# Optimization experiments

Measured on AMD Instinct MI355X. Metric: run time of the kernel, lower is better.

## Reference

```python
import jax, jax.numpy as jnp
import numpy as np

HEADS = 4
NEG_SLOPE = 0.2  # DGL GATConv default leaky_relu slope


def _gat_conv(h, src, dst, W, al, ar, resW, b, heads, out_feats, num_nodes):
    """DGL GATConv semantics with prefix-shape support.
    h: [N, *prefix, in]; returns [N, *prefix, heads, out_feats].
    """
    prefix = h.shape[1:-1]
    z = jnp.einsum('...i,ij->...j', h, W).reshape(h.shape[0], *prefix, heads, out_feats)
    # per-node attention halves: [N, *prefix, heads, 1]
    el = jnp.sum(z * al, axis=-1, keepdims=True)
    er = jnp.sum(z * ar, axis=-1, keepdims=True)
    # per-edge logits: [E, *prefix, heads, 1]
    e = jax.nn.leaky_relu(el[src] + er[dst], NEG_SLOPE)
    # edge softmax over incoming edges of each dst node (stable)
    emax = jax.ops.segment_max(e, dst, num_segments=num_nodes)
    emax = jax.lax.stop_gradient(jnp.where(jnp.isfinite(emax), emax, 0.0))
    ex = jnp.exp(e - emax[dst])
    denom = jax.ops.segment_sum(ex, dst, num_segments=num_nodes)
    a = ex / jnp.where(denom == 0, 1.0, denom)[dst]
    # weighted scatter-aggregate of messages
    rst = jax.ops.segment_sum(z[src] * a, dst, num_segments=num_nodes)
    # residual projection + bias + relu activation
    res = jnp.einsum('...i,ij->...j', h, resW).reshape(h.shape[0], *prefix, heads, out_feats)
    return jax.nn.relu(rst + res + b.reshape(heads, out_feats))


def setup_inputs() -> dict:
    key = jax.random.key(0)
    ks = jax.random.split(key, 16)
    N, E, IN, HID, OUT2, CLS = 8192, 65536, 256, 512, 32, 40
    def w(k, shape, fan_in):
        return jax.random.normal(k, shape, dtype=jnp.float32) * (1.0 / np.sqrt(fan_in))
    return {
        'features': jax.random.normal(ks[0], (N, IN), dtype=jnp.float32),
        'src': jax.random.randint(ks[1], (E,), 0, N, dtype=jnp.int32),
        'dst': jax.random.randint(ks[2], (E,), 0, N, dtype=jnp.int32),
        # layer 1: in=256 -> heads=4, out=512
        'W1': w(ks[3], (IN, HEADS * HID), IN),
        'al1': w(ks[4], (HEADS, HID), HID),
        'ar1': w(ks[5], (HEADS, HID), HID),
        'resW1': w(ks[6], (IN, HEADS * HID), IN),
        'b1': jnp.zeros((HEADS * HID,), dtype=jnp.float32),
        # layer 2: in=512 -> heads=4, out=32 (applied per prefix head dim)
        'W2': w(ks[7], (HID, HEADS * OUT2), HID),
        'al2': w(ks[8], (HEADS, OUT2), OUT2),
        'ar2': w(ks[9], (HEADS, OUT2), OUT2),
        'resW2': w(ks[10], (HID, HEADS * OUT2), HID),
        'b2': jnp.zeros((HEADS * OUT2,), dtype=jnp.float32),
        # final linear: 32*4^2 = 512 -> 40
        'Wout': w(ks[11], (OUT2 * HEADS * HEADS, CLS), OUT2 * HEADS * HEADS),
        'bout': jnp.zeros((CLS,), dtype=jnp.float32),
    }


def reference(features, src, dst, W1, al1, ar1, resW1, b1, W2, al2, ar2, resW2, b2, Wout, bout):
    N = features.shape[0]
    # dropout is identity at inference
    h1 = _gat_conv(features, src, dst, W1, al1, ar1, resW1, b1, HEADS, 512, N)  # [N,4,512]
    h2 = _gat_conv(h1, src, dst, W2, al2, ar2, resW2, b2, HEADS, 32, N)        # [N,4,4,32]
    h = h2.reshape(N, -1)  # [N,512]
    return h @ Wout + bout
```

## Files before the change

### kernel.cpp

```cpp
#include <hip/hip_runtime.h>
#include <cmath>

constexpr int IN_F  = 256;

typedef short bf16x8 __attribute__((ext_vector_type(8)));
typedef short short4v __attribute__((ext_vector_type(4)));
typedef float f32x4 __attribute__((ext_vector_type(4)));

__device__ __forceinline__ short f2bf(float f) {
    unsigned u = __float_as_uint(f);
    unsigned r = (u + 0x7FFFu + ((u >> 16) & 1)) >> 16;
    return (short)r;
}
__device__ __forceinline__ float b2f(short s) {
    return __uint_as_float(((unsigned)(unsigned short)s) << 16);
}

__device__ __forceinline__ int xcd_logical_id()
{
    int nx = gridDim.x, ny = gridDim.y, nz = gridDim.z;
    int flat = blockIdx.x + nx * (blockIdx.y + ny * blockIdx.z);
    int nwg = nx * ny * nz;
    if (nwg & 7) return flat;
    int chunk = nwg >> 3;
    return (flat & 7) * chunk + (flat >> 3);
}

__device__ __forceinline__ void cvt_t_body(
    const float* __restrict__ W, short* __restrict__ Wt, int K, int N,
    int ldwt, int koff, int bk, int bn, int tx, int ty)
{
    __shared__ float tile[32][33];
    for (int i = ty; i < 32; i += 8) {
        int gn = bn + tx;
        tile[i][tx] = (gn < N) ? W[(size_t)(bk + i) * N + gn] : 0.f;
    }
    __syncthreads();
    for (int i = ty; i < 32; i += 8)
        Wt[(size_t)(bn + i) * ldwt + koff + bk + tx] = f2bf(tile[tx][i]);
}

__global__ __launch_bounds__(256) void prep_all(
    const float* __restrict__ W1, const float* __restrict__ al1, const float* __restrict__ ar1,
    const float* __restrict__ resW1, const float* __restrict__ resW2,
    const float* __restrict__ W2, const float* __restrict__ Wout, const float* __restrict__ b2,
    short* __restrict__ Wcomb, short* __restrict__ W2comb, short* __restrict__ Wtout,
    float* __restrict__ wal1, float* __restrict__ war1,
    float* __restrict__ bias2c, int* __restrict__ zero_base)
{
    int bid = blockIdx.x;
    int t   = threadIdx.x;
    if (bid < 256) {
        int wid  = (bid * 256 + t) >> 6;
        int lane = t & 63;
        int k = wid >> 2, h = wid & 3;
        const float* wr  = W1  + (size_t)k * 2048 + h * 512;
        const float* alp = al1 + h * 512;
        const float* arp = ar1 + h * 512;
        float sl = 0.f, sr = 0.f;
        for (int j = lane; j < 512; j += 64) {
            float wv = wr[j];
            sl = fmaf(wv, alp[j], sl);
            sr = fmaf(wv, arp[j], sr);
        }
#pragma unroll
        for (int o = 32; o; o >>= 1) { sl += __shfl_down(sl, o); sr += __shfl_down(sr, o); }
        if (lane == 0) { wal1[wid] = sl; war1[wid] = sr; }
    } else if (bid < 1280) {
        int id = bid - 256;
        int bx = id & 63, by = (id >> 6) & 7, bz = id >> 9;
        const float* W = bz ? resW1 : W1;
        cvt_t_body(W, Wcomb, 256, 2048, 512, bz ? 256 : 0,
                   by * 32, bx * 32, t & 31, t >> 5);
    } else if (bid < 1472) {
        int id = bid - 1280;
        int bx = id & 3, by = (id >> 2) & 15, bz = id >> 6;
        const float* W; short* Wt; int N;
        if (bz == 0)      { W = W2;    Wt = W2comb;             N = 128; }
        else if (bz == 1) { W = resW2; Wt = W2comb + 128 * 512; N = 128; }
        else              { W = Wout;  Wt = Wtout;              N = 40;  }
        cvt_t_body(W, Wt, 512, N, 512, 0, by * 32, bx * 32, t & 31, t >> 5);
    } else if (bid == 1472) {
        bias2c[t] = (t < 128) ? 0.f : b2[t - 128];
    } else {
        int b = bid - 1473;
        int4 z; z.x = 0; z.y = 0; z.z = 0; z.w = 0;
        ((int4*)zero_base)[(size_t)b * 256 + t] = z;
    }
}

__global__ __launch_bounds__(256) void l1_front(
    const float* __restrict__ feat, const float4* __restrict__ wal, const float4* __restrict__ war,
    short* __restrict__ featb, float* __restrict__ el, float* __restrict__ er,
    const int* __restrict__ dst, int* __restrict__ deg, int E, int nfeat)
{
    if ((int)blockIdx.x >= nfeat) {
        int e = (blockIdx.x - nfeat) * 256 + threadIdx.x;
        if (e < E) atomicAdd(&deg[dst[e]], 1);
        return;
    }
    int row  = blockIdx.x * 4 + (threadIdx.x >> 6);
    int lane = threadIdx.x & 63;
    float4 v = ((const float4*)feat)[(size_t)row * 64 + lane];
    short4v o;
    o[0] = f2bf(v.x); o[1] = f2bf(v.y); o[2] = f2bf(v.z); o[3] = f2bf(v.w);
    *(short4v*)(featb + (size_t)row * 256 + lane * 4) = o;

    float fj[4] = { v.x, v.y, v.z, v.w };
    int k = lane * 4;
    float sl[4] = {}, sr[4] = {};
#pragma unroll
    for (int j = 0; j < 4; j++) {
        float4 wl = wal[k + j], wr = war[k + j];
        sl[0] = fmaf(fj[j], wl.x, sl[0]); sl[1] = fmaf(fj[j], wl.y, sl[1]);
        sl[2] = fmaf(fj[j], wl.z, sl[2]); sl[3] = fmaf(fj[j], wl.w, sl[3]);
        sr[0] = fmaf(fj[j], wr.x, sr[0]); sr[1] = fmaf(fj[j], wr.y, sr[1]);
        sr[2] = fmaf(fj[j], wr.z, sr[2]); sr[3] = fmaf(fj[j], wr.w, sr[3]);
    }
#pragma unroll
    for (int o2 = 32; o2; o2 >>= 1) {
#pragma unroll
        for (int h = 0; h < 4; h++) { sl[h] += __shfl_down(sl[h], o2); sr[h] += __shfl_down(sr[h], o2); }
    }
    if (lane == 0) {
#pragma unroll
        for (int h = 0; h < 4; h++) { el[row * 4 + h] = sl[h]; er[row * 4 + h] = sr[h]; }
    }
}

__global__ __launch_bounds__(256) void el2_from_z2(
    const short* __restrict__ z2res, const float* __restrict__ al2, const float* __restrict__ ar2,
    float* __restrict__ el, float* __restrict__ er)
{
    int m    = blockIdx.x * 4 + (threadIdx.x >> 6);
    int lane = threadIdx.x & 63;
    unsigned zv = *(const unsigned*)(z2res + (size_t)m * 256 + lane * 2);
    float z0 = b2f((short)(zv & 0xFFFFu)), z1 = b2f((short)(zv >> 16));
    int c = lane >> 4;
    int j = (lane & 15) * 2;
    float sl = fmaf(z1, al2[c * 32 + j + 1], z0 * al2[c * 32 + j]);
    float sr = fmaf(z1, ar2[c * 32 + j + 1], z0 * ar2[c * 32 + j]);
#pragma unroll
    for (int o = 8; o; o >>= 1) { sl += __shfl_xor(sl, o); sr += __shfl_xor(sr, o); }
    if ((lane & 15) == 0) { el[m * 4 + c] = sl; er[m * 4 + c] = sr; }
}

__global__ __launch_bounds__(256) void gemm_bf16(
    const short* __restrict__ A, const short* __restrict__ Bt,
    const float* __restrict__ bias, void* __restrict__ C,
    int M, int N, int K, int ldc, int nmax, int out_bf16)
{
    __shared__ short sA[2][128 * 32];
    __shared__ short sB[2][128 * 32];
    const int tid  = threadIdx.x;
    const int wave = tid >> 6, lane = tid & 63;
    const int wm = wave >> 1, wn = wave & 1;
    int lid = xcd_logical_id();
    const int bx = lid % gridDim.x, by = lid / gridDim.x;
    const int m0 = by * 128, n0 = bx * 128;

    const int srow = tid >> 2;
    const int scol = (tid & 3) * 8;
    const int fr = lane & 15;
    const int fq = lane >> 4;

    f32x4 acc[4][4] = {};

    for (int k0 = 0; k0 < K; k0 += 64) {
#pragma unroll
        for (int hh = 0; hh < 2; hh++) {
            int kc = k0 + hh * 32 + scol;
            const short* ga0 = A  + (size_t)(m0 + srow) * K + kc;
            const short* ga1 = A  + (size_t)(m0 + 64 + srow) * K + kc;
            const short* gb0 = Bt + (size_t)(n0 + srow) * K + kc;
            const short* gb1 = Bt + (size_t)(n0 + 64 + srow) * K + kc;
            __builtin_amdgcn_global_load_lds((const __attribute__((address_space(1))) void*)ga0,
                (__attribute__((address_space(3))) void*)(sA[hh] + wave * 512), 16, 0, 0);
            __builtin_amdgcn_global_load_lds((const __attribute__((address_space(1))) void*)ga1,
                (__attribute__((address_space(3))) void*)(sA[hh] + 2048 + wave * 512), 16, 0, 0);
            __builtin_amdgcn_global_load_lds((const __attribute__((address_space(1))) void*)gb0,
                (__attribute__((address_space(3))) void*)(sB[hh] + wave * 512), 16, 0, 0);
            __builtin_amdgcn_global_load_lds((const __attribute__((address_space(1))) void*)gb1,
                (__attribute__((address_space(3))) void*)(sB[hh] + 2048 + wave * 512), 16, 0, 0);
        }
        __syncthreads();

#pragma unroll
        for (int hh = 0; hh < 2; hh++) {
            bf16x8 af[4], bfr[4];
#pragma unroll
            for (int m = 0; m < 4; m++)
                af[m] = *(const bf16x8*)(sA[hh] + (wm * 64 + m * 16 + fr) * 32 + fq * 8);
#pragma unroll
            for (int n = 0; n < 4; n++)
                bfr[n] = *(const bf16x8*)(sB[hh] + (wn * 64 + n * 16 + fr) * 32 + fq * 8);
#pragma unroll
            for (int m = 0; m < 4; m++)
#pragma unroll
                for (int n = 0; n < 4; n++)
                    acc[m][n] = __builtin_amdgcn_mfma_f32_16x16x32_bf16(af[m], bfr[n], acc[m][n], 0, 0, 0);
        }
        __syncthreads();
    }

#pragma unroll
    for (int n = 0; n < 4; n++) {
        int gcol = n0 + wn * 64 + n * 16 + fr;
        if (gcol >= nmax) continue;
        float bv = bias ? bias[gcol] : 0.f;
#pragma unroll
        for (int m = 0; m < 4; m++) {
#pragma unroll
            for (int j = 0; j < 4; j++) {
                int grow = m0 + wm * 64 + m * 16 + fq * 4 + j;
                float v = acc[m][n][j] + bv;
                if (out_bf16) ((short*)C)[(size_t)grow * ldc + gcol] = f2bf(v);
                else          ((float*)C)[(size_t)grow * ldc + gcol] = v;
            }
        }
    }
}

__global__ __launch_bounds__(256) void gemm_h1(
    const short* __restrict__ Acomb, const short* __restrict__ Wcomb,
    const float* __restrict__ b1, short* __restrict__ h1b)
{
    __shared__ short sA[2][128 * 32];
    __shared__ short sB[2][128 * 32];
    const int tid  = threadIdx.x;
    const int wave = tid >> 6, lane = tid & 63;
    const int wm = wave >> 1, wn = wave & 1;
    int lid = xcd_logical_id();
    const int bx = lid & 3;
    const int by = (lid >> 2) % gridDim.y;
    const int h  = lid / (gridDim.y * 4);
    const int m0 = by * 128, n0 = bx * 128;
    const short* A  = Acomb + h * 512;
    const short* Bt = Wcomb + (size_t)(h * 512) * 512;

    const int srow = tid >> 2;
    const int scol = (tid & 3) * 8;
    const int fr = lane & 15;
    const int fq = lane >> 4;

    f32x4 acc[4][4] = {};

    for (int k0 = 0; k0 < 512; k0 += 64) {
#pragma unroll
        for (int hh = 0; hh < 2; hh++) {
            int kc = k0 + hh * 32 + scol;
            const short* ga0 = A  + (size_t)(m0 + srow) * 2048 + kc;
            const short* ga1 = A  + (size_t)(m0 + 64 + srow) * 2048 + kc;
            const short* gb0 = Bt + (size_t)(n0 + srow) * 512 + kc;
            const short* gb1 = Bt + (size_t)(n0 + 64 + srow) * 512 + kc;
            __builtin_amdgcn_global_load_lds((const __attribute__((address_space(1))) void*)ga0,
                (__attribute__((address_space(3))) void*)(sA[hh] + wave * 512), 16, 0, 0);
            __builtin_amdgcn_global_load_lds((const __attribute__((address_space(1))) void*)ga1,
                (__attribute__((address_space(3))) void*)(sA[hh] + 2048 + wave * 512), 16, 0, 0);
            __builtin_amdgcn_global_load_lds((const __attribute__((address_space(1))) void*)gb0,
                (__attribute__((address_space(3))) void*)(sB[hh] + wave * 512), 16, 0, 0);
            __builtin_amdgcn_global_load_lds((const __attribute__((address_space(1))) void*)gb1,
                (__attribute__((address_space(3))) void*)(sB[hh] + 2048 + wave * 512), 16, 0, 0);
        }
        __syncthreads();

#pragma unroll
        for (int hh = 0; hh < 2; hh++) {
            bf16x8 af[4], bfr[4];
#pragma unroll
            for (int m = 0; m < 4; m++)
                af[m] = *(const bf16x8*)(sA[hh] + (wm * 64 + m * 16 + fr) * 32 + fq * 8);
#pragma unroll
            for (int n = 0; n < 4; n++)
                bfr[n] = *(const bf16x8*)(sB[hh] + (wn * 64 + n * 16 + fr) * 32 + fq * 8);
#pragma unroll
            for (int m = 0; m < 4; m++)
#pragma unroll
                for (int n = 0; n < 4; n++)
                    acc[m][n] = __builtin_amdgcn_mfma_f32_16x16x32_bf16(af[m], bfr[n], acc[m][n], 0, 0, 0);
        }
        __syncthreads();
    }

#pragma unroll
    for (int n = 0; n < 4; n++) {
        int gcol = h * 512 + n0 + wn * 64 + n * 16 + fr;
        float bv = b1[gcol];
#pragma unroll
        for (int m = 0; m < 4; m++) {
#pragma unroll
            for (int j = 0; j < 4; j++) {
                int grow = m0 + wm * 64 + m * 16 + fq * 4 + j;
                float v = acc[m][n][j] + bv;
                h1b[(size_t)grow * 2048 + gcol] = f2bf(v > 0.f ? v : 0.f);
            }
        }
    }
}

__global__ __launch_bounds__(1024) void scan_excl(const int* __restrict__ deg,
                                                  int* __restrict__ off, int N)
{
    __shared__ int part[1024];
    int t = threadIdx.x;
    int chunk = N >> 10;
    int base = t * chunk;
    int local[16];
    int s = 0;
    for (int i = 0; i < chunk; i++) { local[i] = s; s += deg[base + i]; }
    part[t] = s;
    __syncthreads();
    for (int o = 1; o < 1024; o <<= 1) {
        int v = (t >= o) ? part[t - o] : 0;
        __syncthreads();
        part[t] += v;
        __syncthreads();
    }
    int pre = (t == 0) ? 0 : part[t - 1];
    for (int i = 0; i < chunk; i++) off[base + i] = pre + local[i];
    if (t == 1023) off[N] = pre + s;
}

__global__ void scatter_kernel(const int* __restrict__ dst, const int* __restrict__ off,
                               int* __restrict__ cur, int* __restrict__ eid, int E)
{
    int e = blockIdx.x * blockDim.x + threadIdx.x;
    if (e < E) {
        int d = dst[e];
        int p = off[d] + atomicAdd(&cur[d], 1);
        eid[p] = e;
    }
}

__global__ __launch_bounds__(256) void aggregate_feat_sm(
    const int* __restrict__ off, const int* __restrict__ eid, const int* __restrict__ src,
    const float* __restrict__ el, const float* __restrict__ er,
    const short* __restrict__ featb, short* __restrict__ Acomb)
{
    int wv = threadIdx.x >> 6, lane = threadIdx.x & 63;
    int n = blockIdx.x * 4 + wv;
    int k4 = lane * 4;
    float4 erv = ((const float4*)er)[n];
    float acc[4][4] = {};
    float accd[4] = {};
    int beg = off[n], end = off[n + 1];
    for (int j = beg; j < end; ++j) {
        int e = eid[j];
        int s = src[e];
        float4 elv = ((const float4*)el)[s];
        float a0 = elv.x + erv.x, a1 = elv.y + erv.y, a2 = elv.z + erv.z, a3 = elv.w + erv.w;
        a0 = __expf(a0 > 0.f ? a0 : 0.2f * a0);
        a1 = __expf(a1 > 0.f ? a1 : 0.2f * a1);
        a2 = __expf(a2 > 0.f ? a2 : 0.2f * a2);
        a3 = __expf(a3 > 0.f ? a3 : 0.2f * a3);
        accd[0] += a0; accd[1] += a1; accd[2] += a2; accd[3] += a3;
        short4v fv = *(const short4v*)(featb + (size_t)s * 256 + k4);
        float f0 = b2f(fv[0]), f1 = b2f(fv[1]), f2 = b2f(fv[2]), f3 = b2f(fv[3]);
        acc[0][0] = fmaf(a0, f0, acc[0][0]); acc[0][1] = fmaf(a0, f1, acc[0][1]);
        acc[0][2] = fmaf(a0, f2, acc[0][2]); acc[0][3] = fmaf(a0, f3, acc[0][3]);
        acc[1][0] = fmaf(a1, f0, acc[1][0]); acc[1][1] = fmaf(a1, f1, acc[1][1]);
        acc[1][2] = fmaf(a1, f2, acc[1][2]); acc[1][3] = fmaf(a1, f3, acc[1][3]);
        acc[2][0] = fmaf(a2, f0, acc[2][0]); acc[2][1] = fmaf(a2, f1, acc[2][1]);
        acc[2][2] = fmaf(a2, f2, acc[2][2]); acc[2][3] = fmaf(a2, f3, acc[2][3]);
        acc[3][0] = fmaf(a3, f0, acc[3][0]); acc[3][1] = fmaf(a3, f1, acc[3][1]);
        acc[3][2] = fmaf(a3, f2, acc[3][2]); acc[3][3] = fmaf(a3, f3, acc[3][3]);
    }
    float inv[4];
#pragma unroll
    for (int h = 0; h < 4; h++) inv[h] = 1.f / (accd[h] == 0.f ? 1.f : accd[h]);
    short4v selfv = *(const short4v*)(featb + (size_t)n * 256 + k4);
#pragma unroll
    for (int h = 0; h < 4; h++) {
        short4v o;
#pragma unroll
        for (int kk = 0; kk < 4; kk++) o[kk] = f2bf(acc[h][kk] * inv[h]);
        *(short4v*)(Acomb + (size_t)n * 2048 + h * 512 + k4) = o;
        *(short4v*)(Acomb + (size_t)n * 2048 + h * 512 + 256 + k4) = selfv;
    }
}

__global__ __launch_bounds__(256) void aggregate2_sm(
    const int* __restrict__ off, const int* __restrict__ eid, const int* __restrict__ src,
    const float* __restrict__ el, const float* __restrict__ er,
    const short* __restrict__ z2res, short* __restrict__ h2)
{
    int n = blockIdx.x, t = threadIdx.x;
    int c = t >> 4;
    int p = t >> 6;
    int rem = (2 * t) & 127;
    float erv = er[n * 16 + c];
    float r0 = 0.f, r1 = 0.f, dn = 0.f;
    int beg = off[n], end = off[n + 1];
    for (int j = beg; j < end; ++j) {
        int e = eid[j];
        int s = src[e];
        float lv = el[s * 16 + c] + erv;
        float a = __expf(lv > 0.f ? lv : 0.2f * lv);
        dn += a;
        unsigned zv = *(const unsigned*)(z2res + ((size_t)s * 4 + p) * 256 + rem);
        r0 = fmaf(a, b2f((short)(zv & 0xFFFFu)), r0);
        r1 = fmaf(a, b2f((short)(zv >> 16)), r1);
    }
    if (dn == 0.f) dn = 1.f;
    float inv = 1.f / dn;
    unsigned rv = *(const unsigned*)(z2res + ((size_t)n * 4 + p) * 256 + 128 + rem);
    float v0 = r0 * inv + b2f((short)(rv & 0xFFFFu));
    float v1 = r1 * inv + b2f((short)(rv >> 16));
    v0 = v0 > 0.f ? v0 : 0.f;
    v1 = v1 > 0.f ? v1 : 0.f;
    unsigned o = ((unsigned)(unsigned short)f2bf(v1) << 16) | (unsigned)(unsigned short)f2bf(v0);
    *(unsigned*)(h2 + (size_t)n * 512 + t * 2) = o;
}

extern "C" void kernel_launch(void* const* d_in, const int* in_sizes, int n_in,
                              void* d_out, int out_size, void* d_ws, size_t ws_size,
                              hipStream_t stream)
{
    const float* feat  = (const float*)d_in[0];
    const int*   src   = (const int*)d_in[1];
    const int*   dst   = (const int*)d_in[2];
    const float* W1    = (const float*)d_in[3];
    const float* al1   = (const float*)d_in[4];
    const float* ar1   = (const float*)d_in[5];
    const float* resW1 = (const float*)d_in[6];
    const float* b1    = (const float*)d_in[7];
    const float* W2    = (const float*)d_in[8];
    const float* al2   = (const float*)d_in[9];
    const float* ar2   = (const float*)d_in[10];
    const float* resW2 = (const float*)d_in[11];
    const float* b2    = (const float*)d_in[12];
    const float* Wout  = (const float*)d_in[13];
    const float* bout  = (const float*)d_in[14];
    const int N = in_sizes[0] / IN_F;
    const int E = in_sizes[1];

    char* w = (char*)d_ws;
    auto alloc = [&](size_t bytes) -> char* {
        char* p = w;
        w += (bytes + 255) & ~(size_t)255;
        return p;
    };
    short*    Acomb   = (short*)alloc((size_t)N * 2048 * 2);
    short*    h1b     = (short*)alloc((size_t)N * 2048 * 2);
    short*    featb   = (short*)alloc((size_t)N * 256 * 2);
    short*    Wcomb   = (short*)alloc((size_t)2048 * 512 * 2);
    short*    W2comb  = (short*)alloc((size_t)256 * 512 * 2);
    short*    Wtout   = (short*)alloc((size_t)128 * 512 * 2);
    float*    bias2c  = (float*)alloc((size_t)256 * 4);
    float*    wal1    = (float*)alloc((size_t)256 * 4 * 4);
    float*    war1    = (float*)alloc((size_t)256 * 4 * 4);
    float*    el1     = (float*)alloc((size_t)N * 4 * 4);
    float*    er1     = (float*)alloc((size_t)N * 4 * 4);
    int*      deg     = (int*)alloc((size_t)N * 4);
    int*      cur     = (int*)alloc((size_t)N * 4);
    int*      off     = (int*)alloc((size_t)(N + 1) * 4);
    int*      eid     = (int*)alloc((size_t)E * 4);
    short*    z2res   = (short*)alloc((size_t)N * 4 * 256 * 2);
    short*    h2b     = (short*)alloc((size_t)N * 512 * 2);
    float*    el2     = (float*)alloc((size_t)N * 16 * 4);
    float*    er2     = (float*)alloc((size_t)N * 16 * 4);

    dim3 blk(256);

    prep_all<<<dim3(1489), blk, 0, stream>>>(W1, al1, ar1, resW1, resW2, W2, Wout, b2,
                                             Wcomb, W2comb, Wtout,
                                             wal1, war1, bias2c, deg);

    l1_front<<<dim3(N / 4 + E / 256), blk, 0, stream>>>(feat, (const float4*)wal1, (const float4*)war1,
                                                        featb, el1, er1, dst, deg, E, N / 4);
    scan_excl<<<dim3(1), dim3(1024), 0, stream>>>(deg, off, N);
    scatter_kernel<<<dim3((E + 255) / 256), blk, 0, stream>>>(dst, off, cur, eid, E);

    aggregate_feat_sm<<<dim3(N / 4), blk, 0, stream>>>(off, eid, src, el1, er1, featb, Acomb);
    gemm_h1<<<dim3(4, N / 128, 4), blk, 0, stream>>>(Acomb, Wcomb, b1, h1b);

    gemm_bf16<<<dim3(2, (N * 4) / 128), blk, 0, stream>>>(h1b, W2comb, bias2c, z2res,
                                                          N * 4, 256, 512, 256, 256, 1);
    el2_from_z2<<<dim3(N), blk, 0, stream>>>(z2res, al2, ar2, el2, er2);
    aggregate2_sm<<<dim3(N), blk, 0, stream>>>(off, eid, src, el2, er2, z2res, h2b);

    gemm_bf16<<<dim3(1, N / 128), blk, 0, stream>>>(h2b, Wtout, bout, (float*)d_out,
                                                    N, 128, 512, 40, 40, 0);
}
```

Before: 147.6 us.

## Fuse layer-2 attention logits into GEMM epilogue and drop duplicated self features

Removes the separate el2_from_z2 kernel by computing the layer-2 el/er dot products from the GEMM accumulators (fp32, before bf16 rounding) with intra-row shuffles in the first column block. Also stops copying self features into the combined A buffer four times per node: gemm_h1 now reads the residual half of K directly from featb, which shrinks the Acomb buffer and the writes in the aggregate kernel. The cost is a longer GEMM epilogue on half the blocks and branching address selection in the load loop.

```diff
diff --git a/kernel.cpp b/kernel.cpp
--- a/kernel.cpp
+++ b/kernel.cpp
@@ -128,27 +128,12 @@
     }
 }
 
-__global__ __launch_bounds__(256) void el2_from_z2(
-    const short* __restrict__ z2res, const float* __restrict__ al2, const float* __restrict__ ar2,
-    float* __restrict__ el, float* __restrict__ er)
-{
-    int m    = blockIdx.x * 4 + (threadIdx.x >> 6);
-    int lane = threadIdx.x & 63;
-    unsigned zv = *(const unsigned*)(z2res + (size_t)m * 256 + lane * 2);
-    float z0 = b2f((short)(zv & 0xFFFFu)), z1 = b2f((short)(zv >> 16));
-    int c = lane >> 4;
-    int j = (lane & 15) * 2;
-    float sl = fmaf(z1, al2[c * 32 + j + 1], z0 * al2[c * 32 + j]);
-    float sr = fmaf(z1, ar2[c * 32 + j + 1], z0 * ar2[c * 32 + j]);
-#pragma unroll
-    for (int o = 8; o; o >>= 1) { sl += __shfl_xor(sl, o); sr += __shfl_xor(sr, o); }
-    if ((lane & 15) == 0) { el[m * 4 + c] = sl; er[m * 4 + c] = sr; }
-}
-
 __global__ __launch_bounds__(256) void gemm_bf16(
     const short* __restrict__ A, const short* __restrict__ Bt,
     const float* __restrict__ bias, void* __restrict__ C,
-    int M, int N, int K, int ldc, int nmax, int out_bf16)
+    int M, int N, int K, int ldc, int nmax, int out_bf16,
+    float* __restrict__ el2, float* __restrict__ er2,
+    const float* __restrict__ al2, const float* __restrict__ ar2, int do_el)
 {
     __shared__ short sA[2][128 * 32];
     __shared__ short sB[2][128 * 32];
@@ -203,6 +188,39 @@
         __syncthreads();
     }
 
+    if (do_el && bx == 0) {
+        float cal[4], car[4];
+#pragma unroll
+        for (int n = 0; n < 4; n++) {
+            cal[n] = al2[wn * 64 + n * 16 + fr];
+            car[n] = ar2[wn * 64 + n * 16 + fr];
+        }
+#pragma unroll
+        for (int m = 0; m < 4; m++) {
+#pragma unroll
+            for (int j = 0; j < 4; j++) {
+                float ell = acc[m][0][j] * cal[0] + acc[m][1][j] * cal[1];
+                float elh = acc[m][2][j] * cal[2] + acc[m][3][j] * cal[3];
+                float erl = acc[m][0][j] * car[0] + acc[m][1][j] * car[1];
+                float erh = acc[m][2][j] * car[2] + acc[m][3][j] * car[3];
+#pragma unroll
+                for (int o = 1; o < 16; o <<= 1) {
+                    ell += __shfl_xor(ell, o);
+                    elh += __shfl_xor(elh, o);
+                    erl += __shfl_xor(erl, o);
+                    erh += __shfl_xor(erh, o);
+                }
+                if (fr == 0) {
+                    int R = m0 + wm * 64 + m * 16 + fq * 4 + j;
+                    el2[R * 4 + wn * 2]     = ell;
+                    el2[R * 4 + wn * 2 + 1] = elh;
+                    er2[R * 4 + wn * 2]     = erl;
+                    er2[R * 4 + wn * 2 + 1] = erh;
+                }
+            }
+        }
+    }
+
 #pragma unroll
     for (int n = 0; n < 4; n++) {
         int gcol = n0 + wn * 64 + n * 16 + fr;
@@ -222,8 +240,8 @@
 }
 
 __global__ __launch_bounds__(256) void gemm_h1(
-    const short* __restrict__ Acomb, const short* __restrict__ Wcomb,
-    const float* __restrict__ b1, short* __restrict__ h1b)
+    const short* __restrict__ Acomb, const short* __restrict__ featb,
+    const short* __restrict__ Wcomb, const float* __restrict__ b1, short* __restrict__ h1b)
 {
     __shared__ short sA[2][128 * 32];
     __shared__ short sB[2][128 * 32];
@@ -235,7 +253,6 @@
     const int by = (lid >> 2) % gridDim.y;
     const int h  = lid / (gridDim.y * 4);
     const int m0 = by * 128, n0 = bx * 128;
-    const short* A  = Acomb + h * 512;
     const short* Bt = Wcomb + (size_t)(h * 512) * 512;
 
     const int srow = tid >> 2;
@@ -246,11 +263,19 @@
     f32x4 acc[4][4] = {};
 
     for (int k0 = 0; k0 < 512; k0 += 64) {
+        const int res_half = (k0 >= 256);
 #pragma unroll
         for (int hh = 0; hh < 2; hh++) {
             int kc = k0 + hh * 32 + scol;
-            const short* ga0 = A  + (size_t)(m0 + srow) * 2048 + kc;
-            const short* ga1 = A  + (size_t)(m0 + 64 + srow) * 2048 + kc;
+            const short* ga0;
+            const short* ga1;
+            if (!res_half) {
+                ga0 = Acomb + ((size_t)(m0 + srow) * 4 + h) * 256 + kc;
+                ga1 = Acomb + ((size_t)(m0 + 64 + srow) * 4 + h) * 256 + kc;
+            } else {
+                ga0 = featb + (size_t)(m0 + srow) * 256 + (kc - 256);
+                ga1 = featb + (size_t)(m0 + 64 + srow) * 256 + (kc - 256);
+            }
             const short* gb0 = Bt + (size_t)(n0 + srow) * 512 + kc;
             const short* gb1 = Bt + (size_t)(n0 + 64 + srow) * 512 + kc;
             __builtin_amdgcn_global_load_lds((const __attribute__((address_space(1))) void*)ga0,
@@ -368,14 +393,12 @@
     float inv[4];
 #pragma unroll
     for (int h = 0; h < 4; h++) inv[h] = 1.f / (accd[h] == 0.f ? 1.f : accd[h]);
-    short4v selfv = *(const short4v*)(featb + (size_t)n * 256 + k4);
 #pragma unroll
     for (int h = 0; h < 4; h++) {
         short4v o;
 #pragma unroll
         for (int kk = 0; kk < 4; kk++) o[kk] = f2bf(acc[h][kk] * inv[h]);
-        *(short4v*)(Acomb + (size_t)n * 2048 + h * 512 + k4) = o;
-        *(short4v*)(Acomb + (size_t)n * 2048 + h * 512 + 256 + k4) = selfv;
+        *(short4v*)(Acomb + ((size_t)n * 4 + h) * 256 + k4) = o;
     }
 }
 
@@ -440,7 +463,7 @@
         w += (bytes + 255) & ~(size_t)255;
         return p;
     };
-    short*    Acomb   = (short*)alloc((size_t)N * 2048 * 2);
+    short*    Acomb   = (short*)alloc((size_t)N * 4 * 256 * 2);
     short*    h1b     = (short*)alloc((size_t)N * 2048 * 2);
     short*    featb   = (short*)alloc((size_t)N * 256 * 2);
     short*    Wcomb   = (short*)alloc((size_t)2048 * 512 * 2);
@@ -472,13 +495,14 @@
     scatter_kernel<<<dim3((E + 255) / 256), blk, 0, stream>>>(dst, off, cur, eid, E);
 
     aggregate_feat_sm<<<dim3(N / 4), blk, 0, stream>>>(off, eid, src, el1, er1, featb, Acomb);
-    gemm_h1<<<dim3(4, N / 128, 4), blk, 0, stream>>>(Acomb, Wcomb, b1, h1b);
+    gemm_h1<<<dim3(4, N / 128, 4), blk, 0, stream>>>(Acomb, featb, Wcomb, b1, h1b);
 
     gemm_bf16<<<dim3(2, (N * 4) / 128), blk, 0, stream>>>(h1b, W2comb, bias2c, z2res,
-                                                          N * 4, 256, 512, 256, 256, 1);
-    el2_from_z2<<<dim3(N), blk, 0, stream>>>(z2res, al2, ar2, el2, er2);
+                                                          N * 4, 256, 512, 256, 256, 1,
+                                                          el2, er2, al2, ar2, 1);
     aggregate2_sm<<<dim3(N), blk, 0, stream>>>(off, eid, src, el2, er2, z2res, h2b);
 
     gemm_bf16<<<dim3(1, N / 128), blk, 0, stream>>>(h2b, Wtout, bout, (float*)d_out,
-                                                    N, 128, 512, 40, 40, 0);
-}
+                                                    N, 128, 512, 40, 40, 0,
+                                                    nullptr, nullptr, nullptr, nullptr, 0);
+}
```

New measurement: 143.7 us. 2.6% less time.
